# Kernel optimization log

Hardware: AMD Instinct MI355X
Metric: run time of the kernel (lower is better)

The kernel has to match this reference:

```python
import jax, jax.numpy as jnp
import numpy as np

H = 256

def setup_inputs() -> dict:
    key = jax.random.key(0)
    ks = jax.random.split(key, 9)
    s = 1.0 / np.sqrt(H)
    x = jax.random.normal(ks[0], (8, 2048, H), dtype=jnp.float32)
    Wq = jax.random.uniform(ks[1], (H, H), jnp.float32, -s, s)
    bq = jax.random.uniform(ks[2], (H,), jnp.float32, -s, s)
    Wk = jax.random.uniform(ks[3], (H, H), jnp.float32, -s, s)
    bk = jax.random.uniform(ks[4], (H,), jnp.float32, -s, s)
    Wv = jax.random.uniform(ks[5], (H, H), jnp.float32, -s, s)
    bv = jax.random.uniform(ks[6], (H,), jnp.float32, -s, s)
    Ww = jax.random.uniform(ks[7], (H, 1), jnp.float32, -s, s)
    bw = jax.random.uniform(ks[8], (1,), jnp.float32, -s, s)
    return {"x": x, "Wq": Wq, "bq": bq, "Wk": Wk, "bk": bk,
            "Wv": Wv, "bv": bv, "Ww": Ww, "bw": bw}

def reference(x, Wq, bq, Wk, bk, Wv, bv, Ww, bw):
    # x: (B, N, H) — cross-asset attention over N assets
    q = x @ Wq + bq
    k = x @ Wk + bk
    v = x @ Wv + bv
    scale = 1.0 / jnp.sqrt(jnp.asarray(q.shape[-1], q.dtype))
    beta = jnp.einsum('bnd,bmd->bnm', q, k) * scale  # (B, N, N)
    beta = jax.nn.softmax(beta, axis=-1)
    # original: sum(value[:,None] * beta[...,None], dim=2) == beta @ v
    out = jnp.einsum('bnm,bmd->bnd', beta, v)
    final_scores = (out @ Ww + bw)[..., 0]  # (B, N)
    return final_scores
```

## Files before the change

kernel.cpp:

```cpp
#include <hip/hip_runtime.h>

#define H 256
#define NB 2048
#define BATCH 8
#define NSPLIT 8
#define KSPAN (NB / NSPLIT)
#define NITER (KSPAN / 64)

typedef unsigned short u16;
using bf16x8 = __attribute__((ext_vector_type(8))) __bf16;
using f32x4  = __attribute__((ext_vector_type(4))) float;

typedef const __attribute__((address_space(1))) void gv_t;
typedef __attribute__((address_space(3))) void lv_t;

__device__ __forceinline__ void gl_lds16(const void* g, void* l) {
    __builtin_amdgcn_global_load_lds((gv_t*)g, (lv_t*)l, 16, 0, 0);
}

#define MFMA(a, b, c) __builtin_amdgcn_mfma_f32_16x16x32_bf16(a, b, c, 0, 0, 0)

__device__ __forceinline__ u16 f2bf(float f) {
    union { float f; unsigned u; } v; v.f = f;
    unsigned r = v.u + 0x7fffu + ((v.u >> 16) & 1u);
    return (u16)(r >> 16);
}

__global__ __launch_bounds__(256) void wprep_kernel(
        const float* __restrict__ Wq, const float* __restrict__ Wk,
        const float* __restrict__ Wv, const float* __restrict__ Ww,
        const float* __restrict__ bq,
        u16* __restrict__ wqb, u16* __restrict__ wkb,
        float* __restrict__ wvw, float* __restrict__ kbv) {
    int f = blockIdx.x, t = threadIdx.x;
    float wq = Wq[f * H + t];
    wqb[f * H + t] = f2bf(wq);
    float wk = Wk[f * H + t];
    wkb[f * H + t] = f2bf(wk);
    float p = Wv[f * H + t] * Ww[t];
    float r = wk * bq[t];
    for (int o = 32; o; o >>= 1) { p += __shfl_xor(p, o); r += __shfl_xor(r, o); }
    __shared__ float redp[4], redr[4];
    int w = t >> 6, lane = t & 63;
    if (lane == 0) { redp[w] = p; redr[w] = r; }
    __syncthreads();
    if (t == 0) {
        wvw[f] = redp[0] + redp[1] + redp[2] + redp[3];
        kbv[f] = redr[0] + redr[1] + redr[2] + redr[3];
    }
}

__global__ __launch_bounds__(256) void prep2_kernel(
        const u16* __restrict__ wkb, const u16* __restrict__ wqb,
        u16* __restrict__ aTb,
        const float* __restrict__ x, const float* __restrict__ wvw,
        const float* __restrict__ kbv, const float* __restrict__ bv,
        const float* __restrict__ Ww,
        u16* __restrict__ xbf, float2* __restrict__ uee) {
    __shared__ u16 bt[16384];
    int id = blockIdx.x, tid = threadIdx.x;

    if (id < 8) {
        int mb = (id >> 2) * 128, nb = (id & 3) * 64;
        int w = tid >> 6, lane = tid & 63;
        int l15 = lane & 15, quad = lane >> 4;

        {
            const u16* gsrc = wqb + (nb + w * 16 + l15) * H + quad * 8;
            for (int ks = 0; ks < 8; ++ks)
                gl_lds16(gsrc + ks * 32, bt + (w * 8 + ks) * 512);
        }

        bf16x8 a[2][8];
        for (int mi = 0; mi < 2; ++mi) {
            const u16* abase = wkb + (size_t)(mb + w * 32 + mi * 16 + l15) * H + quad * 8;
            for (int ks = 0; ks < 8; ++ks) a[mi][ks] = *(const bf16x8*)(abase + ks * 32);
        }
        __syncthreads();

        f32x4 acc[2][4] = {};
        for (int ks = 0; ks < 8; ++ks)
            for (int t = 0; t < 4; ++t) {
                bf16x8 b = *(const bf16x8*)(bt + ((t * 8 + ks) * 64 + lane) * 8);
                acc[0][t] = MFMA(a[0][ks], b, acc[0][t]);
                acc[1][t] = MFMA(a[1][ks], b, acc[1][t]);
            }

        for (int mi = 0; mi < 2; ++mi) {
            int m = mb + w * 32 + mi * 16 + quad * 4;
            for (int t = 0; t < 4; ++t) {
                int n = nb + t * 16 + l15;
                for (int r = 0; r < 4; ++r)
                    aTb[(size_t)(m + r) * H + n] = f2bf(acc[mi][t][r] * 0.0625f);
            }
        }
        return;
    }

    int lane = tid & 63;
    int row  = (id - 8) * 4 + (tid >> 6);
    float4 xv = *(const float4*)(x + row * H + lane * 4);
    ushort4 o;
    o.x = f2bf(xv.x); o.y = f2bf(xv.y); o.z = f2bf(xv.z); o.w = f2bf(xv.w);
    *(ushort4*)(xbf + row * H + lane * 4) = o;
    float4 wv = *(const float4*)(wvw + lane * 4);
    float s = xv.x * wv.x + xv.y * wv.y + xv.z * wv.z + xv.w * wv.w;
    float4 kv = *(const float4*)(kbv + lane * 4);
    float d = xv.x * kv.x + xv.y * kv.y + xv.z * kv.z + xv.w * kv.w;
    float4 bvv = *(const float4*)(bv + lane * 4);
    float4 www = *(const float4*)(Ww + lane * 4);
    float c = bvv.x * www.x + bvv.y * www.y + bvv.z * www.z + bvv.w * www.w;
    for (int o2 = 32; o2; o2 >>= 1) {
        s += __shfl_xor(s, o2); d += __shfl_xor(d, o2); c += __shfl_xor(c, o2);
    }
    if (lane == 0) {
        float e = __expf(d * 0.0625f);
        uee[row] = make_float2(e * (s + c), e);
    }
}

__global__ __launch_bounds__(256) void gemm_bt_kernel(
        const u16* __restrict__ A, const u16* __restrict__ B,
        u16* __restrict__ C, float scale) {
    __shared__ u16 bt[16384];
    int tid = threadIdx.x;
    int mb = blockIdx.x * 128, nb = blockIdx.y * 64;
    int w = tid >> 6, lane = tid & 63;
    int l15 = lane & 15, quad = lane >> 4;

    {
        const u16* gsrc = B + (nb + w * 16 + l15) * H + quad * 8;
        for (int ks = 0; ks < 8; ++ks)
            gl_lds16(gsrc + ks * 32, bt + (w * 8 + ks) * 512);
    }

    bf16x8 a[2][8];
    for (int mi = 0; mi < 2; ++mi) {
        const u16* abase = A + (size_t)(mb + w * 32 + mi * 16 + l15) * H + quad * 8;
        for (int ks = 0; ks < 8; ++ks) a[mi][ks] = *(const bf16x8*)(abase + ks * 32);
    }
    __syncthreads();

    f32x4 acc[2][4] = {};
    for (int ks = 0; ks < 8; ++ks)
        for (int t = 0; t < 4; ++t) {
            bf16x8 b = *(const bf16x8*)(bt + ((t * 8 + ks) * 64 + lane) * 8);
            acc[0][t] = MFMA(a[0][ks], b, acc[0][t]);
            acc[1][t] = MFMA(a[1][ks], b, acc[1][t]);
        }

    for (int mi = 0; mi < 2; ++mi) {
        int m = mb + w * 32 + mi * 16 + quad * 4;
        for (int t = 0; t < 4; ++t) {
            int n = nb + t * 16 + l15;
            for (int r = 0; r < 4; ++r)
                C[(size_t)(m + r) * H + n] = f2bf(acc[mi][t][r] * scale);
        }
    }
}

__global__ __launch_bounds__(256, 2) void attn_kernel(
        const u16* __restrict__ T, const u16* __restrict__ xbf,
        const float2* __restrict__ uee,
        float* __restrict__ pnum, float* __restrict__ pden) {
    __shared__ u16 kt[32768];
    int tid = threadIdx.x;
    int id = blockIdx.x;
    int b = id & 7, rest = id >> 3;
    int qc = rest & 7, sp = rest >> 3;
    int w = tid >> 6, lane = tid & 63, l15 = lane & 15, quad = lane >> 4;
    int qb = qc * 256;

    bf16x8 aq[4][8];
    {
        const u16* qbase = T + (size_t)(b * NB + qb + w * 64 + l15) * H + quad * 8;
        #pragma unroll
        for (int mi = 0; mi < 4; ++mi)
            #pragma unroll
            for (int ks = 0; ks < 8; ++ks)
                aq[mi][ks] = *(const bf16x8*)(qbase + mi * 16 * H + ks * 32);
    }

    const u16* xb = xbf + (size_t)b * NB * H;
    const float2* uep = uee + (size_t)b * NB;
    const int kb0 = sp * KSPAN;

    const u16* gsrc = xb + (size_t)(kb0 + w * 16 + l15) * H + quad * 8;
    #pragma unroll
    for (int j = 0; j < 8; ++j)
        gl_lds16(gsrc + j * 32, kt + (w * 8 + j) * 512);
    __syncthreads();

    float ls[4][4] = {}, as_[4][4] = {};

    #pragma unroll 1
    for (int h = 0; h < NITER; ++h) {
        const u16* ktc = kt + (h & 1) * 16384;
        if (h + 1 < NITER) {
            u16* dst = kt + ((h & 1) ^ 1) * 16384;
            const u16* g2 = gsrc + (size_t)(h + 1) * 64 * H;
            #pragma unroll
            for (int j = 0; j < 8; ++j)
                gl_lds16(g2 + j * 32, dst + (w * 8 + j) * 512);
        }
        int kb64 = kb0 + h * 64;
        float2 uv[4];
        #pragma unroll
        for (int t = 0; t < 4; ++t) uv[t] = uep[kb64 + t * 16 + l15];

        #pragma unroll
        for (int t = 0; t < 4; ++t) {
            f32x4 acc[4] = {};
            #pragma unroll
            for (int ks = 0; ks < 8; ++ks) {
                bf16x8 bfr = *(const bf16x8*)(ktc + ((t * 8 + ks) * 64 + lane) * 8);
                acc[0] = MFMA(aq[0][ks], bfr, acc[0]);
                acc[1] = MFMA(aq[1][ks], bfr, acc[1]);
                acc[2] = MFMA(aq[2][ks], bfr, acc[2]);
                acc[3] = MFMA(aq[3][ks], bfr, acc[3]);
            }
            #pragma unroll
            for (int mi = 0; mi < 4; ++mi)
                #pragma unroll
                for (int r = 0; r < 4; ++r) {
                    float p = __expf(acc[mi][r]);
                    as_[mi][r] += p * uv[t].x;
                    ls[mi][r]  += p * uv[t].y;
                }
        }
        __syncthreads();
    }

    #pragma unroll
    for (int mi = 0; mi < 4; ++mi)
        #pragma unroll
        for (int r = 0; r < 4; ++r)
            for (int o = 1; o < 16; o <<= 1) {
                ls[mi][r]  += __shfl_xor(ls[mi][r], o);
                as_[mi][r] += __shfl_xor(as_[mi][r], o);
            }

    if (l15 == 0) {
        size_t base = (size_t)(sp * BATCH + b) * NB + qb + w * 64 + quad * 4;
        #pragma unroll
        for (int mi = 0; mi < 4; ++mi)
            #pragma unroll
            for (int r = 0; r < 4; ++r) {
                pnum[base + mi * 16 + r] = as_[mi][r];
                pden[base + mi * 16 + r] = ls[mi][r];
            }
    }
}

__global__ __launch_bounds__(256) void finalize_kernel(
        const float* __restrict__ pnum, const float* __restrict__ pden,
        const float* __restrict__ bw, float* __restrict__ out) {
    int i = blockIdx.x * 256 + threadIdx.x;
    float num = 0.f, den = 0.f;
    for (int sp = 0; sp < NSPLIT; ++sp) {
        num += pnum[sp * (BATCH * NB) + i];
        den += pden[sp * (BATCH * NB) + i];
    }
    out[i] = num / den + bw[0];
}

extern "C" void kernel_launch(void* const* d_in, const int* in_sizes, int n_in,
                              void* d_out, int out_size, void* d_ws, size_t ws_size,
                              hipStream_t stream) {
    (void)in_sizes; (void)n_in; (void)out_size; (void)ws_size;
    const float* x  = (const float*)d_in[0];
    const float* Wq = (const float*)d_in[1];
    const float* bq = (const float*)d_in[2];
    const float* Wk = (const float*)d_in[3];
    const float* bk = (const float*)d_in[4];  (void)bk;
    const float* Wv = (const float*)d_in[5];
    const float* bv = (const float*)d_in[6];
    const float* Ww = (const float*)d_in[7];
    const float* bw = (const float*)d_in[8];
    float* out = (float*)d_out;

    u16* xbf = (u16*)d_ws;
    u16* Tbf = xbf + 4194304;
    u16* aTb = Tbf + 4194304;
    u16* wqb = aTb + 65536;
    u16* wkb = wqb + 65536;
    float* wvw = (float*)(wkb + 65536);
    float* kbv = wvw + 256;
    float2* uee = (float2*)(kbv + 256);
    float* pnum = (float*)(uee + 16384);
    float* pden = pnum + NSPLIT * BATCH * NB;

    hipLaunchKernelGGL(wprep_kernel, dim3(256), dim3(256), 0, stream,
                       Wq, Wk, Wv, Ww, bq, wqb, wkb, wvw, kbv);
    hipLaunchKernelGGL(prep2_kernel, dim3(4104), dim3(256), 0, stream,
                       wkb, wqb, aTb, x, wvw, kbv, bv, Ww, xbf, uee);
    hipLaunchKernelGGL(gemm_bt_kernel, dim3(128, 4), dim3(256), 0, stream,
                       xbf, aTb, Tbf, 1.0f);
    hipLaunchKernelGGL(attn_kernel, dim3(8 * 8 * NSPLIT), dim3(256), 0, stream,
                       Tbf, xbf, uee, pnum, pden);
    hipLaunchKernelGGL(finalize_kernel, dim3(64), dim3(256), 0, stream,
                       pnum, pden, bw, out);
}
```

Before: 122.9 us.

## Merge weight prep kernels and move per-row score vectors into the T GEMM

```diff
diff --git a/kernel.cpp b/kernel.cpp
--- a/kernel.cpp
+++ b/kernel.cpp
@@ -26,37 +26,23 @@
     return (u16)(r >> 16);
 }
 
-__global__ __launch_bounds__(256) void wprep_kernel(
+__device__ __forceinline__ bf16x8 cvt8(const float* p) {
+    float4 f0 = *(const float4*)p;
+    float4 f1 = *(const float4*)(p + 4);
+    union { bf16x8 v; u16 u[8]; } r;
+    r.u[0] = f2bf(f0.x); r.u[1] = f2bf(f0.y); r.u[2] = f2bf(f0.z); r.u[3] = f2bf(f0.w);
+    r.u[4] = f2bf(f1.x); r.u[5] = f2bf(f1.y); r.u[6] = f2bf(f1.z); r.u[7] = f2bf(f1.w);
+    return r.v;
+}
+
+__global__ __launch_bounds__(256) void prepA_kernel(
         const float* __restrict__ Wq, const float* __restrict__ Wk,
         const float* __restrict__ Wv, const float* __restrict__ Ww,
-        const float* __restrict__ bq,
-        u16* __restrict__ wqb, u16* __restrict__ wkb,
-        float* __restrict__ wvw, float* __restrict__ kbv) {
-    int f = blockIdx.x, t = threadIdx.x;
-    float wq = Wq[f * H + t];
-    wqb[f * H + t] = f2bf(wq);
-    float wk = Wk[f * H + t];
-    wkb[f * H + t] = f2bf(wk);
-    float p = Wv[f * H + t] * Ww[t];
-    float r = wk * bq[t];
-    for (int o = 32; o; o >>= 1) { p += __shfl_xor(p, o); r += __shfl_xor(r, o); }
-    __shared__ float redp[4], redr[4];
-    int w = t >> 6, lane = t & 63;
-    if (lane == 0) { redp[w] = p; redr[w] = r; }
-    __syncthreads();
-    if (t == 0) {
-        wvw[f] = redp[0] + redp[1] + redp[2] + redp[3];
-        kbv[f] = redr[0] + redr[1] + redr[2] + redr[3];
-    }
-}
-
-__global__ __launch_bounds__(256) void prep2_kernel(
-        const u16* __restrict__ wkb, const u16* __restrict__ wqb,
-        u16* __restrict__ aTb,
-        const float* __restrict__ x, const float* __restrict__ wvw,
-        const float* __restrict__ kbv, const float* __restrict__ bv,
-        const float* __restrict__ Ww,
-        u16* __restrict__ xbf, float2* __restrict__ uee) {
+        const float* __restrict__ bq, const float* __restrict__ bv,
+        const float* __restrict__ x,
+        u16* __restrict__ aTb, float* __restrict__ wvw,
+        float* __restrict__ kbv, float* __restrict__ ccp,
+        u16* __restrict__ xbf) {
     __shared__ u16 bt[16384];
     int id = blockIdx.x, tid = threadIdx.x;
 
@@ -66,65 +52,82 @@
         int l15 = lane & 15, quad = lane >> 4;
 
         {
-            const u16* gsrc = wqb + (nb + w * 16 + l15) * H + quad * 8;
+            const float* src = Wq + (nb + w * 16 + l15) * H + quad * 8;
+            #pragma unroll
             for (int ks = 0; ks < 8; ++ks)
-                gl_lds16(gsrc + ks * 32, bt + (w * 8 + ks) * 512);
+                *(bf16x8*)(bt + (w * 8 + ks) * 512 + lane * 8) = cvt8(src + ks * 32);
         }
 
         bf16x8 a[2][8];
+        #pragma unroll
         for (int mi = 0; mi < 2; ++mi) {
-            const u16* abase = wkb + (size_t)(mb + w * 32 + mi * 16 + l15) * H + quad * 8;
-            for (int ks = 0; ks < 8; ++ks) a[mi][ks] = *(const bf16x8*)(abase + ks * 32);
+            const float* ab = Wk + (mb + w * 32 + mi * 16 + l15) * H + quad * 8;
+            #pragma unroll
+            for (int ks = 0; ks < 8; ++ks) a[mi][ks] = cvt8(ab + ks * 32);
         }
         __syncthreads();
 
         f32x4 acc[2][4] = {};
+        #pragma unroll
         for (int ks = 0; ks < 8; ++ks)
-            for (int t = 0; t < 4; ++t) {
-                bf16x8 b = *(const bf16x8*)(bt + ((t * 8 + ks) * 64 + lane) * 8);
-                acc[0][t] = MFMA(a[0][ks], b, acc[0][t]);
-                acc[1][t] = MFMA(a[1][ks], b, acc[1][t]);
-            }
-
+            #pragma unroll
+            for (int tt = 0; tt < 4; ++tt) {
+                bf16x8 b = *(const bf16x8*)(bt + ((tt * 8 + ks) * 64 + lane) * 8);
+                acc[0][tt] = MFMA(a[0][ks], b, acc[0][tt]);
+                acc[1][tt] = MFMA(a[1][ks], b, acc[1][tt]);
+            }
+
+        #pragma unroll
         for (int mi = 0; mi < 2; ++mi) {
             int m = mb + w * 32 + mi * 16 + quad * 4;
-            for (int t = 0; t < 4; ++t) {
-                int n = nb + t * 16 + l15;
-                for (int r = 0; r < 4; ++r)
-                    aTb[(size_t)(m + r) * H + n] = f2bf(acc[mi][t][r] * 0.0625f);
+            #pragma unroll
+            for (int tt = 0; tt < 4; ++tt) {
+                int n = nb + tt * 16 + l15;
+                #pragma unroll
+                for (int r2 = 0; r2 < 4; ++r2)
+                    aTb[(size_t)(m + r2) * H + n] = f2bf(acc[mi][tt][r2] * 0.0625f);
             }
         }
         return;
     }
 
+    if (id < 264) {
+        int f = id - 8, t = tid;
+        float p = Wv[f * H + t] * Ww[t];
+        float r = Wk[f * H + t] * bq[t];
+        float c = (f == 0) ? bv[t] * Ww[t] : 0.f;
+        for (int o = 32; o; o >>= 1) {
+            p += __shfl_xor(p, o); r += __shfl_xor(r, o); c += __shfl_xor(c, o);
+        }
+        __shared__ float redp[4], redr[4], redc[4];
+        int w = t >> 6, lane = t & 63;
+        if (lane == 0) { redp[w] = p; redr[w] = r; redc[w] = c; }
+        __syncthreads();
+        if (t == 0) {
+            wvw[f] = redp[0] + redp[1] + redp[2] + redp[3];
+            kbv[f] = redr[0] + redr[1] + redr[2] + redr[3];
+            if (f == 0) ccp[0] = redc[0] + redc[1] + redc[2] + redc[3];
+        }
+        return;
+    }
+
     int lane = tid & 63;
-    int row  = (id - 8) * 4 + (tid >> 6);
-    float4 xv = *(const float4*)(x + row * H + lane * 4);
+    int row  = (id - 264) * 4 + (tid >> 6);
+    float4 xv = *(const float4*)(x + (size_t)row * H + lane * 4);
     ushort4 o;
     o.x = f2bf(xv.x); o.y = f2bf(xv.y); o.z = f2bf(xv.z); o.w = f2bf(xv.w);
-    *(ushort4*)(xbf + row * H + lane * 4) = o;
-    float4 wv = *(const float4*)(wvw + lane * 4);
-    float s = xv.x * wv.x + xv.y * wv.y + xv.z * wv.z + xv.w * wv.w;
-    float4 kv = *(const float4*)(kbv + lane * 4);
-    float d = xv.x * kv.x + xv.y * kv.y + xv.z * kv.z + xv.w * kv.w;
-    float4 bvv = *(const float4*)(bv + lane * 4);
-    float4 www = *(const float4*)(Ww + lane * 4);
-    float c = bvv.x * www.x + bvv.y * www.y + bvv.z * www.z + bvv.w * www.w;
-    for (int o2 = 32; o2; o2 >>= 1) {
-        s += __shfl_xor(s, o2); d += __shfl_xor(d, o2); c += __shfl_xor(c, o2);
-    }
-    if (lane == 0) {
-        float e = __expf(d * 0.0625f);
-        uee[row] = make_float2(e * (s + c), e);
-    }
-}
-
-__global__ __launch_bounds__(256) void gemm_bt_kernel(
+    *(ushort4*)(xbf + (size_t)row * H + lane * 4) = o;
+}
+
+__global__ __launch_bounds__(256) void gemmTu_kernel(
         const u16* __restrict__ A, const u16* __restrict__ B,
-        u16* __restrict__ C, float scale) {
+        u16* __restrict__ C,
+        const float* __restrict__ x, const float* __restrict__ wvw,
+        const float* __restrict__ kbv, const float* __restrict__ ccp,
+        float2* __restrict__ uee) {
     __shared__ u16 bt[16384];
     int tid = threadIdx.x;
-    int mb = blockIdx.x * 128, nb = blockIdx.y * 64;
+    int mb = blockIdx.x * 128, nbI = blockIdx.y, nb = nbI * 64;
     int w = tid >> 6, lane = tid & 63;
     int l15 = lane & 15, quad = lane >> 4;
 
@@ -138,6 +141,27 @@
     for (int mi = 0; mi < 2; ++mi) {
         const u16* abase = A + (size_t)(mb + w * 32 + mi * 16 + l15) * H + quad * 8;
         for (int ks = 0; ks < 8; ++ks) a[mi][ks] = *(const bf16x8*)(abase + ks * 32);
+    }
+
+    {
+        int rbase = mb + nbI * 32 + w * 8;
+        float cc = ccp[0];
+        float4 wv = *(const float4*)(wvw + lane * 4);
+        float4 kv = *(const float4*)(kbv + lane * 4);
+        #pragma unroll
+        for (int rr = 0; rr < 8; ++rr) {
+            int row = rbase + rr;
+            float4 xv = *(const float4*)(x + (size_t)row * H + lane * 4);
+            float s = xv.x * wv.x + xv.y * wv.y + xv.z * wv.z + xv.w * wv.w;
+            float d = xv.x * kv.x + xv.y * kv.y + xv.z * kv.z + xv.w * kv.w;
+            for (int o2 = 32; o2; o2 >>= 1) {
+                s += __shfl_xor(s, o2); d += __shfl_xor(d, o2);
+            }
+            if (lane == 0) {
+                float e = __expf(d * 0.0625f);
+                uee[row] = make_float2(e * (s + cc), e);
+            }
+        }
     }
     __syncthreads();
 
@@ -154,7 +178,7 @@
         for (int t = 0; t < 4; ++t) {
             int n = nb + t * 16 + l15;
             for (int r = 0; r < 4; ++r)
-                C[(size_t)(m + r) * H + n] = f2bf(acc[mi][t][r] * scale);
+                C[(size_t)(m + r) * H + n] = f2bf(acc[mi][t][r]);
         }
     }
 }
@@ -282,20 +306,17 @@
     u16* xbf = (u16*)d_ws;
     u16* Tbf = xbf + 4194304;
     u16* aTb = Tbf + 4194304;
-    u16* wqb = aTb + 65536;
-    u16* wkb = wqb + 65536;
-    float* wvw = (float*)(wkb + 65536);
+    float* wvw = (float*)(aTb + 65536);
     float* kbv = wvw + 256;
-    float2* uee = (float2*)(kbv + 256);
+    float* ccp = kbv + 256;
+    float2* uee = (float2*)(ccp + 4);
     float* pnum = (float*)(uee + 16384);
     float* pden = pnum + NSPLIT * BATCH * NB;
 
-    hipLaunchKernelGGL(wprep_kernel, dim3(256), dim3(256), 0, stream,
-                       Wq, Wk, Wv, Ww, bq, wqb, wkb, wvw, kbv);
-    hipLaunchKernelGGL(prep2_kernel, dim3(4104), dim3(256), 0, stream,
-                       wkb, wqb, aTb, x, wvw, kbv, bv, Ww, xbf, uee);
-    hipLaunchKernelGGL(gemm_bt_kernel, dim3(128, 4), dim3(256), 0, stream,
-                       xbf, aTb, Tbf, 1.0f);
+    hipLaunchKernelGGL(prepA_kernel, dim3(4360), dim3(256), 0, stream,
+                       Wq, Wk, Wv, Ww, bq, bv, x, aTb, wvw, kbv, ccp, xbf);
+    hipLaunchKernelGGL(gemmTu_kernel, dim3(128, 4), dim3(256), 0, stream,
+                       xbf, aTb, Tbf, x, wvw, kbv, ccp, uee);
     hipLaunchKernelGGL(attn_kernel, dim3(8 * 8 * NSPLIT), dim3(256), 0, stream,
                        Tbf, xbf, uee, pnum, pden);
     hipLaunchKernelGGL(finalize_kernel, dim3(64), dim3(256), 0, stream,
```

Result: slower. 126.7 us (+3.1%).
